# Performance work log

Measured on AMD Instinct MI355X. Metric: run time of the kernel, lower is better.

Reference implementation:

```python
import jax, jax.numpy as jnp
import numpy as np

B, S, H, HEADS = 4, 4096, 256, 4
DH = H // HEADS
WINDOW = 16
N = B * S
EPS = 1e-5


def _build_edges():
    half = WINDOW // 2
    i = np.arange(S)
    offs = np.concatenate([np.arange(-half, 0), np.arange(1, half)])  # j in [i-half, i+half), j != i
    j = i[:, None] + offs[None, :]
    valid = (j >= 0) & (j < S)
    src_i = np.broadcast_to(i[:, None], j.shape)[valid]
    tgt_j = j[valid]
    w = (1.0 / (1.0 + np.abs(src_i - tgt_j))).astype(np.float32)
    boff = np.arange(B)[:, None] * S
    src = (boff + src_i[None, :]).reshape(-1).astype(np.int32)
    tgt = (boff + tgt_j[None, :]).reshape(-1).astype(np.int32)
    w = np.tile(w, B)
    return src, tgt, w


def setup_inputs() -> dict:
    key = jax.random.key(0)
    ks = jax.random.split(key, 8)
    src, tgt, w = _build_edges()
    sc = 0.02
    return {
        "hidden_states": jax.random.normal(ks[0], (B, S, H), jnp.float32),
        "Wc": jax.random.normal(ks[1], (H, H), jnp.float32) * sc,
        "bc": jnp.zeros((H,), jnp.float32),
        "Wa": jax.random.normal(ks[2], (H, H), jnp.float32) * sc,
        "a_src": jax.random.normal(ks[3], (HEADS, DH), jnp.float32) * sc,
        "a_tgt": jax.random.normal(ks[4], (HEADS, DH), jnp.float32) * sc,
        "ba": jnp.zeros((H,), jnp.float32),
        "ln_g": jnp.ones((H,), jnp.float32),
        "ln_b": jnp.zeros((H,), jnp.float32),
        "Wg": jax.random.normal(ks[5], (2 * H, H), jnp.float32) * sc,
        "bg": jnp.zeros((H,), jnp.float32),
        "Wp": jax.random.normal(ks[6], (H, H), jnp.float32) * sc,
        "bp": jnp.zeros((H,), jnp.float32),
        "edge_weights": jnp.asarray(w),
        "src": jnp.asarray(src),
        "tgt": jnp.asarray(tgt),
    }


def _ln(x, g, b):
    mu = jnp.mean(x, -1, keepdims=True)
    var = jnp.mean((x - mu) ** 2, -1, keepdims=True)
    return (x - mu) * jax.lax.rsqrt(var + EPS) * g + b


def reference(hidden_states, Wc, bc, Wa, a_src, a_tgt, ba, ln_g, ln_b,
              Wg, bg, Wp, bp, edge_weights, src, tgt):
    x = hidden_states.reshape(N, H)

    # --- layer 0: GraphConvolution ---
    support = x @ Wc                                   # [N,H]
    msg = edge_weights[:, None] * support[src]         # [E,H]
    gs = jax.ops.segment_sum(msg, tgt, num_segments=N) + bc
    gs = _ln(gs + x, ln_g, ln_b)

    # --- layer 1: GraphAttention (GAT-style, edge-weighted softmax) ---
    h = (gs @ Wa).reshape(N, HEADS, DH)
    es = jnp.einsum('nhd,hd->nh', h, a_src)            # [N,heads]
    et = jnp.einsum('nhd,hd->nh', h, a_tgt)
    logits = jax.nn.leaky_relu(es[src] + et[tgt], 0.2)  # [E,heads]
    m = jax.ops.segment_max(logits, tgt, num_segments=N)
    un = jnp.exp(logits - m[tgt]) * edge_weights[:, None]
    den = jax.ops.segment_sum(un, tgt, num_segments=N)
    alpha = un / (den[tgt] + 1e-9)                      # [E,heads]
    agg = jax.ops.segment_sum(alpha[:, :, None] * h[src], tgt, num_segments=N)
    gs = agg.reshape(N, H) + ba
    gs = _ln(gs + x, ln_g, ln_b)

    # --- gated integration ---
    gate = jax.nn.sigmoid(jnp.concatenate([x, gs], -1) @ Wg + bg)
    enhanced = x + gate * (gs @ Wp + bp)
    return enhanced.reshape(B, S, H)
```

## Files before the change

### kernel.cpp

```cpp
#include <hip/hip_runtime.h>
#include <math.h>

#define HD 256
#define SEQ 4096
#define NR 16384
#define NHEADS 4
#define EPSV 1e-5f
#define LDP 72
#define ZLDP 264
#define SROWS 32
#define SHALO 15
#define SLDP 264

typedef __attribute__((ext_vector_type(8))) short bf16x8;
typedef __attribute__((ext_vector_type(4))) float f32x4;

__device__ inline short f2bf(float f) {
    unsigned u = __float_as_uint(f);
    u += 0x7FFF + ((u >> 16) & 1);
    return (short)(u >> 16);
}
__device__ inline float bf2f(short s) {
    return __uint_as_float(((unsigned)(unsigned short)s) << 16);
}

__device__ inline void stage_tile(const short* __restrict__ src, int src_stride,
                                  int row0, int k0, short* lds, int rows)
{
    int t = threadIdx.x;
    int nchunk = rows >> 5;
#pragma unroll
    for (int c = 0; c < 8; ++c) {
        if (c >= nchunk) break;
        int idx = c * 256 + t;
        int r = idx >> 3, kg = idx & 7;
        bf16x8 v = *(const bf16x8*)(src + (size_t)(row0 + r) * src_stride + k0 + kg * 8);
        *(bf16x8*)(lds + r * LDP + kg * 8) = v;
    }
}

__global__ __launch_bounds__(256) void prep_stencil(
    const float* __restrict__ x,
    const float* __restrict__ Wc, const float* __restrict__ Wa,
    const float* __restrict__ Wg, const float* __restrict__ Wp,
    short* __restrict__ xb, short* __restrict__ y,
    short* __restrict__ WcT, short* __restrict__ WaT,
    short* __restrict__ WgT, short* __restrict__ WpT)
{
    __shared__ __align__(16) char smem[(SROWS + SHALO) * SLDP * 2];
    int task = blockIdx.y;
    int bx = blockIdx.x;
    int t = threadIdx.x;

    if (task == 0) {
        short* lH = (short*)smem;
        int t0 = bx * SROWS;
        int batch_base = t0 & ~(SEQ - 1);
        for (int i = t; i < (SROWS + SHALO) * 64; i += 256) {
            int r = i >> 6, c4 = (i & 63) * 4;
            int grow = t0 - 7 + r;
            short4 o4 = {0, 0, 0, 0};
            if (grow >= batch_base && grow < batch_base + SEQ) {
                float4 v = *(const float4*)(x + (size_t)grow * HD + c4);
                o4.x = f2bf(v.x); o4.y = f2bf(v.y); o4.z = f2bf(v.z); o4.w = f2bf(v.w);
            }
            *(short4*)(lH + r * SLDP + c4) = o4;
        }
        __syncthreads();
        for (int i = t; i < SROWS * 64; i += 256) {
            int r = i >> 6, c4 = (i & 63) * 4;
            *(short4*)(xb + (size_t)(t0 + r) * HD + c4) =
                *(const short4*)(lH + (r + 7) * SLDP + c4);
        }
        int wv = t >> 6, lane = t & 63;
        int c0 = lane * 4;
        for (int rr = wv; rr < SROWS; rr += 4) {
            float a0 = 0.f, a1 = 0.f, a2 = 0.f, a3 = 0.f;
#pragma unroll
            for (int i = 0; i < 15; ++i) {
                int d = (i < 7) ? (i - 7) : (i - 6);
                float wd = 1.f / (1.f + (float)((d < 0) ? -d : d));
                short4 s4 = *(const short4*)(lH + (rr + 7 + d) * SLDP + c0);
                a0 += wd * bf2f(s4.x); a1 += wd * bf2f(s4.y);
                a2 += wd * bf2f(s4.z); a3 += wd * bf2f(s4.w);
            }
            short4 o;
            o.x = f2bf(a0); o.y = f2bf(a1); o.z = f2bf(a2); o.w = f2bf(a3);
            *(short4*)(y + (size_t)(t0 + rr) * HD + c0) = o;
        }
        return;
    }
    float (*lds)[65] = (float (*)[65])smem;
    const float* W; short* Wt; int K;
    if (task == 1)      { W = Wc; Wt = WcT; K = 256; }
    else if (task == 2) { W = Wa; Wt = WaT; K = 256; }
    else if (task == 3) { W = Wg; Wt = WgT; K = 512; }
    else                { W = Wp; Wt = WpT; K = 256; }
    int ntiles = (K >> 6) * 4;
    if (bx >= ntiles) return;
    int k0 = (bx >> 2) * 64, n0 = (bx & 3) * 64;
    int ty = t >> 6, tx = t & 63;
#pragma unroll
    for (int s = 0; s < 16; ++s) {
        int r = s * 4 + ty;
        lds[r][tx] = W[(size_t)(k0 + r) * 256 + n0 + tx];
    }
    __syncthreads();
#pragma unroll
    for (int s = 0; s < 16; ++s) {
        int rn = s * 4 + ty;
        Wt[(size_t)(n0 + rn) * K + k0 + tx] = f2bf(lds[tx][rn]);
    }
}

__global__ __launch_bounds__(256) void gemm_fused(
    const short* __restrict__ y, const short* __restrict__ WcT,
    const short* __restrict__ xb, const float* __restrict__ bc,
    const short* __restrict__ WaT,
    const float* __restrict__ lng, const float* __restrict__ lnb,
    const float* __restrict__ a_src, const float* __restrict__ a_tgt,
    short* __restrict__ hb, float* __restrict__ es, float* __restrict__ et)
{
    __shared__ __align__(16) short lA[32 * LDP];
    __shared__ __align__(16) short lB[256 * LDP];
    __shared__ __align__(16) short lZ[32 * ZLDP];
    __shared__ float red_s[2][32], red_q[2][32];
    int t = threadIdx.x;
    int lane = t & 63, wid = t >> 6;
    int wm = wid & 1, wn = wid >> 1;
    int m0 = blockIdx.x * 32;
    int lm = lane & 15, lk = (lane >> 4) * 8;
    int rbase = (lane >> 4) * 4;

    f32x4 acc[8] = {};
    for (int kt = 0; kt < 4; ++kt) {
        __syncthreads();
        {
            int r = t >> 3, kg = t & 7;
            *(bf16x8*)(lA + r * LDP + kg * 8) =
                *(const bf16x8*)(y + (size_t)(m0 + r) * HD + kt * 64 + kg * 8);
        }
        stage_tile(WcT, HD, 0, kt * 64, lB, 256);
        __syncthreads();
#pragma unroll
        for (int kk2 = 0; kk2 < 64; kk2 += 32) {
            bf16x8 a = *(const bf16x8*)(lA + (wm * 16 + lm) * LDP + kk2 + lk);
#pragma unroll
            for (int j = 0; j < 8; ++j) {
                bf16x8 b = *(const bf16x8*)(lB + (wn * 128 + j * 16 + lm) * LDP + kk2 + lk);
                acc[j] = __builtin_amdgcn_mfma_f32_16x16x32_bf16(a, b, acc[j], 0, 0, 0);
            }
        }
    }
    float zv[8][4];
    float s4r[4] = {}, q4r[4] = {};
#pragma unroll
    for (int j = 0; j < 8; ++j)
#pragma unroll
        for (int r = 0; r < 4; ++r) {
            int n = wn * 128 + j * 16 + lm;
            int row = m0 + wm * 16 + rbase + r;
            float z = acc[j][r] + bc[n] + bf2f(xb[(size_t)row * HD + n]);
            zv[j][r] = z; s4r[r] += z; q4r[r] += z * z;
        }
#pragma unroll
    for (int r = 0; r < 4; ++r)
#pragma unroll
        for (int o = 1; o < 16; o <<= 1) {
            s4r[r] += __shfl_xor(s4r[r], o, 64);
            q4r[r] += __shfl_xor(q4r[r], o, 64);
        }
    if (lm == 0)
#pragma unroll
        for (int r = 0; r < 4; ++r) {
            red_s[wn][wm * 16 + rbase + r] = s4r[r];
            red_q[wn][wm * 16 + rbase + r] = q4r[r];
        }
    __syncthreads();
    float mu[4], inv[4];
#pragma unroll
    for (int r = 0; r < 4; ++r) {
        int rowl = wm * 16 + rbase + r;
        float S = red_s[0][rowl] + red_s[1][rowl];
        float Q = red_q[0][rowl] + red_q[1][rowl];
        mu[r] = S * (1.f / HD);
        inv[r] = rsqrtf(Q * (1.f / HD) - mu[r] * mu[r] + EPSV);
    }
#pragma unroll
    for (int j = 0; j < 8; ++j)
#pragma unroll
        for (int r = 0; r < 4; ++r) {
            int n = wn * 128 + j * 16 + lm;
            int rowl = wm * 16 + rbase + r;
            lZ[rowl * ZLDP + n] = f2bf((zv[j][r] - mu[r]) * inv[r] * lng[n] + lnb[n]);
        }

    f32x4 acc2[8] = {};
    for (int kt = 0; kt < 4; ++kt) {
        __syncthreads();
        stage_tile(WaT, HD, 0, kt * 64, lB, 256);
        __syncthreads();
#pragma unroll
        for (int kk2 = 0; kk2 < 64; kk2 += 32) {
            bf16x8 a = *(const bf16x8*)(lZ + (wm * 16 + lm) * ZLDP + kt * 64 + kk2 + lk);
#pragma unroll
            for (int j = 0; j < 8; ++j) {
                bf16x8 b = *(const bf16x8*)(lB + (wn * 128 + j * 16 + lm) * LDP + kk2 + lk);
                acc2[j] = __builtin_amdgcn_mfma_f32_16x16x32_bf16(a, b, acc2[j], 0, 0, 0);
            }
        }
    }
    float esA[4] = {}, etA[4] = {}, esB[4] = {}, etB[4] = {};
#pragma unroll
    for (int j = 0; j < 8; ++j) {
        int n = wn * 128 + j * 16 + lm;
        float as = a_src[n], at = a_tgt[n];
#pragma unroll
        for (int r = 0; r < 4; ++r) {
            int row = m0 + wm * 16 + rbase + r;
            hb[(size_t)row * HD + n] = f2bf(acc2[j][r]);
            if (j < 4) { esA[r] += acc2[j][r] * as; etA[r] += acc2[j][r] * at; }
            else       { esB[r] += acc2[j][r] * as; etB[r] += acc2[j][r] * at; }
        }
    }
#pragma unroll
    for (int r = 0; r < 4; ++r) {
#pragma unroll
        for (int o = 1; o < 16; o <<= 1) {
            esA[r] += __shfl_xor(esA[r], o, 64);
            etA[r] += __shfl_xor(etA[r], o, 64);
            esB[r] += __shfl_xor(esB[r], o, 64);
            etB[r] += __shfl_xor(etB[r], o, 64);
        }
        if (lm == 0) {
            int row = m0 + wm * 16 + rbase + r;
            es[row * NHEADS + wn * 2 + 0] = esA[r];
            et[row * NHEADS + wn * 2 + 0] = etA[r];
            es[row * NHEADS + wn * 2 + 1] = esB[r];
            et[row * NHEADS + wn * 2 + 1] = etB[r];
        }
    }
}

__global__ __launch_bounds__(256) void attn_ln(const short* __restrict__ hb,
                                               const float* __restrict__ es,
                                               const float* __restrict__ et,
                                               const short* __restrict__ xb,
                                               const float* __restrict__ ba,
                                               const float* __restrict__ g,
                                               const float* __restrict__ bb,
                                               short* __restrict__ out)
{
    __shared__ short lH[(SROWS + SHALO) * SLDP];
    int t0 = blockIdx.x * SROWS;
    int batch_base = t0 & ~(SEQ - 1);
    int t = threadIdx.x;
    for (int i = t; i < (SROWS + SHALO) * 64; i += 256) {
        int r = i >> 6, c4 = (i & 63) * 4;
        int grow = t0 - 7 + r;
        short4 v = {0, 0, 0, 0};
        if (grow >= batch_base && grow < batch_base + SEQ)
            v = *(const short4*)(hb + (size_t)grow * HD + c4);
        *(short4*)(lH + r * SLDP + c4) = v;
    }
    __syncthreads();

    int wv = t >> 6, lane = t & 63;
    int tap = lane >> 2, hh = lane & 3;
    int hd = lane >> 4;
    int c0 = lane * 4;
    for (int rr = wv; rr < SROWS; rr += 4) {
        int trow = t0 + rr;
        int p = trow & (SEQ - 1);
        float lg = -1e30f, wd = 0.f;
        bool okk = false;
        if (tap < 15) {
            int d = (tap < 7) ? (tap - 7) : (tap - 6);
            int qp = p + d;
            okk = (qp >= 0) && (qp < SEQ);
            if (okk) {
                float l = es[(trow + d) * NHEADS + hh] + et[trow * NHEADS + hh];
                lg = (l > 0.f) ? l : 0.2f * l;
            }
            wd = 1.f / (1.f + (float)((d < 0) ? -d : d));
        }
        float m = lg;
#pragma unroll
        for (int o = 4; o < 64; o <<= 1) m = fmaxf(m, __shfl_xor(m, o, 64));
        float un = okk ? __expf(lg - m) * wd : 0.f;
        float den = un;
#pragma unroll
        for (int o = 4; o < 64; o <<= 1) den += __shfl_xor(den, o, 64);
        float alpha_l = un / (den + 1e-9f);

        float al[15];
#pragma unroll
        for (int i = 0; i < 15; ++i) al[i] = __shfl(alpha_l, i * 4 + hd, 64);

        float a0 = 0.f, a1 = 0.f, a2 = 0.f, a3 = 0.f;
#pragma unroll
        for (int i = 0; i < 15; ++i) {
            int d = (i < 7) ? (i - 7) : (i - 6);
            short4 s4 = *(const short4*)(lH + (rr + 7 + d) * SLDP + c0);
            a0 += al[i] * bf2f(s4.x); a1 += al[i] * bf2f(s4.y);
            a2 += al[i] * bf2f(s4.z); a3 += al[i] * bf2f(s4.w);
        }
        short4 xv4 = *(const short4*)(xb + (size_t)trow * HD + c0);
        float4 bav = *(const float4*)(ba + c0);
        float v0 = a0 + bav.x + bf2f(xv4.x), v1 = a1 + bav.y + bf2f(xv4.y);
        float v2 = a2 + bav.z + bf2f(xv4.z), v3 = a3 + bav.w + bf2f(xv4.w);
        float s = v0 + v1 + v2 + v3;
        float q = v0 * v0 + v1 * v1 + v2 * v2 + v3 * v3;
#pragma unroll
        for (int o = 1; o < 64; o <<= 1) { s += __shfl_xor(s, o, 64); q += __shfl_xor(q, o, 64); }
        float mu = s * (1.f / HD);
        float var = q * (1.f / HD) - mu * mu;
        float inv = rsqrtf(var + EPSV);
        float4 gv = *(const float4*)(g + c0);
        float4 bv = *(const float4*)(bb + c0);
        short4 o4;
        o4.x = f2bf((v0 - mu) * inv * gv.x + bv.x);
        o4.y = f2bf((v1 - mu) * inv * gv.y + bv.y);
        o4.z = f2bf((v2 - mu) * inv * gv.z + bv.z);
        o4.w = f2bf((v3 - mu) * inv * gv.w + bv.w);
        *(short4*)(out + (size_t)trow * HD + c0) = o4;
    }
}

__global__ __launch_bounds__(256) void final_mfma(const short* __restrict__ xb,
                                                  const short* __restrict__ gs2b,
                                                  const short* __restrict__ WgT,
                                                  const float* __restrict__ bg,
                                                  const short* __restrict__ WpT,
                                                  const float* __restrict__ bp,
                                                  float* __restrict__ out)
{
    __shared__ __align__(16) short lX[64 * LDP];
    __shared__ __align__(16) short lG[64 * LDP];
    __shared__ __align__(16) short lB1[64 * LDP];
    __shared__ __align__(16) short lB2[64 * LDP];
    __shared__ __align__(16) short lB3[64 * LDP];
    int tid = threadIdx.x;
    int lane = tid & 63, wid = tid >> 6;
    int m0 = blockIdx.y * 64;
    int n0 = blockIdx.x * 64;
    int wrow = wid * 16;
    int lm = lane & 15, lk = (lane >> 4) * 8;
    f32x4 accg[4] = {}, accp[4] = {};
    for (int kt = 0; kt < 4; ++kt) {
        int k0 = kt * 64;
        __syncthreads();
        stage_tile(xb,   HD,  m0, k0, lX, 64);
        stage_tile(gs2b, HD,  m0, k0, lG, 64);
        stage_tile(WgT,  512, n0, k0, lB1, 64);
        stage_tile(WgT,  512, n0, k0 + 256, lB2, 64);
        stage_tile(WpT,  HD,  n0, k0, lB3, 64);
        __syncthreads();
#pragma unroll
        for (int kk2 = 0; kk2 < 64; kk2 += 32) {
            int ro = (wrow + lm) * LDP + kk2 + lk;
            bf16x8 ax = *(const bf16x8*)(lX + ro);
            bf16x8 ag = *(const bf16x8*)(lG + ro);
            bf16x8 b1[4], b2[4], b3[4];
#pragma unroll
            for (int j = 0; j < 4; ++j) {
                int rb = (j * 16 + lm) * LDP + kk2 + lk;
                b1[j] = *(const bf16x8*)(lB1 + rb);
                b2[j] = *(const bf16x8*)(lB2 + rb);
                b3[j] = *(const bf16x8*)(lB3 + rb);
            }
#pragma unroll
            for (int j = 0; j < 4; ++j) {
                accg[j] = __builtin_amdgcn_mfma_f32_16x16x32_bf16(ax, b1[j], accg[j], 0, 0, 0);
                accg[j] = __builtin_amdgcn_mfma_f32_16x16x32_bf16(ag, b2[j], accg[j], 0, 0, 0);
                accp[j] = __builtin_amdgcn_mfma_f32_16x16x32_bf16(ag, b3[j], accp[j], 0, 0, 0);
            }
        }
    }
    int rbase = (lane >> 4) * 4;
#pragma unroll
    for (int j = 0; j < 4; ++j)
#pragma unroll
        for (int r = 0; r < 4; ++r) {
            size_t m = (size_t)(m0 + wrow + rbase + r);
            int n = n0 + j * 16 + lm;
            float gate = 1.f / (1.f + __expf(-(accg[j][r] + bg[n])));
            float pv = accp[j][r] + bp[n];
            out[m * HD + n] = bf2f(xb[m * HD + n]) + gate * pv;
        }
}

extern "C" void kernel_launch(void* const* d_in, const int* in_sizes, int n_in,
                              void* d_out, int out_size, void* d_ws, size_t ws_size,
                              hipStream_t stream)
{
    const float* x     = (const float*)d_in[0];
    const float* Wc    = (const float*)d_in[1];
    const float* bc    = (const float*)d_in[2];
    const float* Wa    = (const float*)d_in[3];
    const float* a_src = (const float*)d_in[4];
    const float* a_tgt = (const float*)d_in[5];
    const float* ba    = (const float*)d_in[6];
    const float* ln_g  = (const float*)d_in[7];
    const float* ln_b  = (const float*)d_in[8];
    const float* Wg    = (const float*)d_in[9];
    const float* bg    = (const float*)d_in[10];
    const float* Wp    = (const float*)d_in[11];
    const float* bp    = (const float*)d_in[12];

    float* out = (float*)d_out;
    short* hb  = (short*)d_out;
    char* dsec = (char*)d_out + (size_t)NR * HD * 2;
    float* es  = (float*)dsec;
    float* et  = es + (size_t)NR * NHEADS;

    char* w = (char*)d_ws;
    short* y   = (short*)w;   w += (size_t)NR * HD * 2;
    short* gsb = (short*)w;   w += (size_t)NR * HD * 2;
    short* xb  = (short*)w;   w += (size_t)NR * HD * 2;
    short* WcT = (short*)w;   w += 256 * 256 * 2;
    short* WaT = (short*)w;   w += 256 * 256 * 2;
    short* WpT = (short*)w;   w += 256 * 256 * 2;
    short* WgT = (short*)w;   w += 512 * 256 * 2;

    dim3 ggrid(HD / 64, NR / 64);

    prep_stencil<<<dim3(NR / SROWS, 5), 256, 0, stream>>>(
        x, Wc, Wa, Wg, Wp, xb, y, WcT, WaT, WgT, WpT);
    gemm_fused<<<NR / 32, 256, 0, stream>>>(y, WcT, xb, bc, WaT, ln_g, ln_b,
                                            a_src, a_tgt, hb, es, et);
    attn_ln<<<NR / SROWS, 256, 0, stream>>>(hb, es, et, xb, ba, ln_g, ln_b, gsb);
    final_mfma<<<ggrid, 256, 0, stream>>>(xb, gsb, WgT, bg, WpT, bp, out);
}
```

Baseline: 69.87 us.

## Fuse attention+LayerNorm with gated output GEMM, keeping normalized rows in LDS

Merges the attention/LayerNorm kernel with the final gating GEMM kernel. Each 32-row block keeps its normalized output and its x rows in shared memory, then computes the full 256-column gate and projection GEMMs by staging weight tiles. This removes the bf16 intermediate round-trip through global memory and one kernel launch. In exchange each block re-streams all of Wg and Wp, roughly doubling weight traffic, and runs twelve staged phases each guarded by barriers. Intermediates that previously lived in the output buffer move to workspace, because the output is now written while other blocks are still reading those intermediates.

```diff
diff --git a/kernel.cpp b/kernel.cpp
--- a/kernel.cpp
+++ b/kernel.cpp
@@ -242,19 +242,28 @@
     }
 }
 
-__global__ __launch_bounds__(256) void attn_ln(const short* __restrict__ hb,
-                                               const float* __restrict__ es,
-                                               const float* __restrict__ et,
-                                               const short* __restrict__ xb,
-                                               const float* __restrict__ ba,
-                                               const float* __restrict__ g,
-                                               const float* __restrict__ bb,
-                                               short* __restrict__ out)
+#define AF_LZ_OFF (256 * LDP * 2)
+#define AF_LX_OFF (256 * LDP * 2 + 32 * ZLDP * 2)
+
+__global__ __launch_bounds__(256) void attn_final(
+    const short* __restrict__ hb, const float* __restrict__ es,
+    const float* __restrict__ et, const short* __restrict__ xb,
+    const float* __restrict__ ba, const float* __restrict__ lng,
+    const float* __restrict__ lnb,
+    const short* __restrict__ WgT, const float* __restrict__ bg,
+    const short* __restrict__ WpT, const float* __restrict__ bp,
+    float* __restrict__ out)
 {
-    __shared__ short lH[(SROWS + SHALO) * SLDP];
+    __shared__ __align__(16) char smem[256 * LDP * 2 + 2 * 32 * ZLDP * 2];
+    short* lH = (short*)smem;
+    short* lB = (short*)smem;
+    short* lZ = (short*)(smem + AF_LZ_OFF);
+    short* lX = (short*)(smem + AF_LX_OFF);
+
+    int t = threadIdx.x;
     int t0 = blockIdx.x * SROWS;
     int batch_base = t0 & ~(SEQ - 1);
-    int t = threadIdx.x;
+
     for (int i = t; i < (SROWS + SHALO) * 64; i += 256) {
         int r = i >> 6, c4 = (i & 63) * 4;
         int grow = t0 - 7 + r;
@@ -262,6 +271,10 @@
         if (grow >= batch_base && grow < batch_base + SEQ)
             v = *(const short4*)(hb + (size_t)grow * HD + c4);
         *(short4*)(lH + r * SLDP + c4) = v;
+    }
+    for (int i = t; i < SROWS * 64; i += 256) {
+        int r = i >> 6, c4 = (i & 63) * 4;
+        *(short4*)(lX + r * ZLDP + c4) = *(const short4*)(xb + (size_t)(t0 + r) * HD + c4);
     }
     __syncthreads();
 
@@ -305,7 +318,7 @@
             a0 += al[i] * bf2f(s4.x); a1 += al[i] * bf2f(s4.y);
             a2 += al[i] * bf2f(s4.z); a3 += al[i] * bf2f(s4.w);
         }
-        short4 xv4 = *(const short4*)(xb + (size_t)trow * HD + c0);
+        short4 xv4 = *(const short4*)(lX + rr * ZLDP + c0);
         float4 bav = *(const float4*)(ba + c0);
         float v0 = a0 + bav.x + bf2f(xv4.x), v1 = a1 + bav.y + bf2f(xv4.y);
         float v2 = a2 + bav.z + bf2f(xv4.z), v3 = a3 + bav.w + bf2f(xv4.w);
@@ -316,77 +329,73 @@
         float mu = s * (1.f / HD);
         float var = q * (1.f / HD) - mu * mu;
         float inv = rsqrtf(var + EPSV);
-        float4 gv = *(const float4*)(g + c0);
-        float4 bv = *(const float4*)(bb + c0);
+        float4 gv = *(const float4*)(lng + c0);
+        float4 bv = *(const float4*)(lnb + c0);
         short4 o4;
         o4.x = f2bf((v0 - mu) * inv * gv.x + bv.x);
         o4.y = f2bf((v1 - mu) * inv * gv.y + bv.y);
         o4.z = f2bf((v2 - mu) * inv * gv.z + bv.z);
         o4.w = f2bf((v3 - mu) * inv * gv.w + bv.w);
-        *(short4*)(out + (size_t)trow * HD + c0) = o4;
-    }
-}
-
-__global__ __launch_bounds__(256) void final_mfma(const short* __restrict__ xb,
-                                                  const short* __restrict__ gs2b,
-                                                  const short* __restrict__ WgT,
-                                                  const float* __restrict__ bg,
-                                                  const short* __restrict__ WpT,
-                                                  const float* __restrict__ bp,
-                                                  float* __restrict__ out)
-{
-    __shared__ __align__(16) short lX[64 * LDP];
-    __shared__ __align__(16) short lG[64 * LDP];
-    __shared__ __align__(16) short lB1[64 * LDP];
-    __shared__ __align__(16) short lB2[64 * LDP];
-    __shared__ __align__(16) short lB3[64 * LDP];
-    int tid = threadIdx.x;
-    int lane = tid & 63, wid = tid >> 6;
-    int m0 = blockIdx.y * 64;
-    int n0 = blockIdx.x * 64;
-    int wrow = wid * 16;
+        *(short4*)(lZ + rr * ZLDP + c0) = o4;
+    }
+
+    int wid = t >> 6;
+    int wm = wid & 1, wn = wid >> 1;
     int lm = lane & 15, lk = (lane >> 4) * 8;
-    f32x4 accg[4] = {}, accp[4] = {};
+    int rbase = (lane >> 4) * 4;
+    f32x4 accg[8] = {}, accp[8] = {};
     for (int kt = 0; kt < 4; ++kt) {
-        int k0 = kt * 64;
-        __syncthreads();
-        stage_tile(xb,   HD,  m0, k0, lX, 64);
-        stage_tile(gs2b, HD,  m0, k0, lG, 64);
-        stage_tile(WgT,  512, n0, k0, lB1, 64);
-        stage_tile(WgT,  512, n0, k0 + 256, lB2, 64);
-        stage_tile(WpT,  HD,  n0, k0, lB3, 64);
+        __syncthreads();
+        stage_tile(WgT, 512, 0, kt * 64, lB, 256);
         __syncthreads();
 #pragma unroll
         for (int kk2 = 0; kk2 < 64; kk2 += 32) {
-            int ro = (wrow + lm) * LDP + kk2 + lk;
-            bf16x8 ax = *(const bf16x8*)(lX + ro);
-            bf16x8 ag = *(const bf16x8*)(lG + ro);
-            bf16x8 b1[4], b2[4], b3[4];
-#pragma unroll
-            for (int j = 0; j < 4; ++j) {
-                int rb = (j * 16 + lm) * LDP + kk2 + lk;
-                b1[j] = *(const bf16x8*)(lB1 + rb);
-                b2[j] = *(const bf16x8*)(lB2 + rb);
-                b3[j] = *(const bf16x8*)(lB3 + rb);
-            }
-#pragma unroll
-            for (int j = 0; j < 4; ++j) {
-                accg[j] = __builtin_amdgcn_mfma_f32_16x16x32_bf16(ax, b1[j], accg[j], 0, 0, 0);
-                accg[j] = __builtin_amdgcn_mfma_f32_16x16x32_bf16(ag, b2[j], accg[j], 0, 0, 0);
-                accp[j] = __builtin_amdgcn_mfma_f32_16x16x32_bf16(ag, b3[j], accp[j], 0, 0, 0);
-            }
-        }
-    }
-    int rbase = (lane >> 4) * 4;
-#pragma unroll
-    for (int j = 0; j < 4; ++j)
+            bf16x8 a = *(const bf16x8*)(lX + (wm * 16 + lm) * ZLDP + kt * 64 + kk2 + lk);
+#pragma unroll
+            for (int j = 0; j < 8; ++j) {
+                bf16x8 b = *(const bf16x8*)(lB + (wn * 128 + j * 16 + lm) * LDP + kk2 + lk);
+                accg[j] = __builtin_amdgcn_mfma_f32_16x16x32_bf16(a, b, accg[j], 0, 0, 0);
+            }
+        }
+    }
+    for (int kt = 0; kt < 4; ++kt) {
+        __syncthreads();
+        stage_tile(WgT, 512, 0, 256 + kt * 64, lB, 256);
+        __syncthreads();
+#pragma unroll
+        for (int kk2 = 0; kk2 < 64; kk2 += 32) {
+            bf16x8 a = *(const bf16x8*)(lZ + (wm * 16 + lm) * ZLDP + kt * 64 + kk2 + lk);
+#pragma unroll
+            for (int j = 0; j < 8; ++j) {
+                bf16x8 b = *(const bf16x8*)(lB + (wn * 128 + j * 16 + lm) * LDP + kk2 + lk);
+                accg[j] = __builtin_amdgcn_mfma_f32_16x16x32_bf16(a, b, accg[j], 0, 0, 0);
+            }
+        }
+    }
+    for (int kt = 0; kt < 4; ++kt) {
+        __syncthreads();
+        stage_tile(WpT, HD, 0, kt * 64, lB, 256);
+        __syncthreads();
+#pragma unroll
+        for (int kk2 = 0; kk2 < 64; kk2 += 32) {
+            bf16x8 a = *(const bf16x8*)(lZ + (wm * 16 + lm) * ZLDP + kt * 64 + kk2 + lk);
+#pragma unroll
+            for (int j = 0; j < 8; ++j) {
+                bf16x8 b = *(const bf16x8*)(lB + (wn * 128 + j * 16 + lm) * LDP + kk2 + lk);
+                accp[j] = __builtin_amdgcn_mfma_f32_16x16x32_bf16(a, b, accp[j], 0, 0, 0);
+            }
+        }
+    }
+#pragma unroll
+    for (int j = 0; j < 8; ++j)
 #pragma unroll
         for (int r = 0; r < 4; ++r) {
-            size_t m = (size_t)(m0 + wrow + rbase + r);
-            int n = n0 + j * 16 + lm;
+            int n = wn * 128 + j * 16 + lm;
+            int rowl = wm * 16 + rbase + r;
+            size_t m = (size_t)(t0 + rowl);
             float gate = 1.f / (1.f + __expf(-(accg[j][r] + bg[n])));
             float pv = accp[j][r] + bp[n];
-            out[m * HD + n] = bf2f(xb[m * HD + n]) + gate * pv;
+            out[m * HD + n] = bf2f(lX[rowl * ZLDP + n]) + gate * pv;
         }
 }
 
@@ -409,26 +418,22 @@
     const float* bp    = (const float*)d_in[12];
 
     float* out = (float*)d_out;
-    short* hb  = (short*)d_out;
-    char* dsec = (char*)d_out + (size_t)NR * HD * 2;
-    float* es  = (float*)dsec;
-    float* et  = es + (size_t)NR * NHEADS;
 
     char* w = (char*)d_ws;
     short* y   = (short*)w;   w += (size_t)NR * HD * 2;
-    short* gsb = (short*)w;   w += (size_t)NR * HD * 2;
     short* xb  = (short*)w;   w += (size_t)NR * HD * 2;
+    short* hb  = (short*)w;   w += (size_t)NR * HD * 2;
+    float* es  = (float*)w;   w += (size_t)NR * NHEADS * 4;
+    float* et  = (float*)w;   w += (size_t)NR * NHEADS * 4;
     short* WcT = (short*)w;   w += 256 * 256 * 2;
     short* WaT = (short*)w;   w += 256 * 256 * 2;
     short* WpT = (short*)w;   w += 256 * 256 * 2;
     short* WgT = (short*)w;   w += 512 * 256 * 2;
 
-    dim3 ggrid(HD / 64, NR / 64);
-
     prep_stencil<<<dim3(NR / SROWS, 5), 256, 0, stream>>>(
         x, Wc, Wa, Wg, Wp, xb, y, WcT, WaT, WgT, WpT);
     gemm_fused<<<NR / 32, 256, 0, stream>>>(y, WcT, xb, bc, WaT, ln_g, ln_b,
                                             a_src, a_tgt, hb, es, et);
-    attn_ln<<<NR / SROWS, 256, 0, stream>>>(hb, es, et, xb, ba, ln_g, ln_b, gsb);
-    final_mfma<<<ggrid, 256, 0, stream>>>(xb, gsb, WgT, bg, WpT, bp, out);
-}
+    attn_final<<<NR / SROWS, 256, 0, stream>>>(hb, es, et, xb, ba, ln_g, ln_b,
+                                               WgT, bg, WpT, bp, out);
+}
```

Result: faster. 66.52 us (-4.8%).
